# Kernel tuning notes

Hardware: AMD Instinct MI355X
Metric: run time of the kernel (lower is better)

Reference implementation:

```python
import jax, jax.numpy as jnp
import numpy as np

B, V, T, D, NC = 512, 4, 16, 512, 174
EPS = 1e-5
_edges = np.ones((V, V)) - np.eye(V)
SEND = np.where(_edges)[0]   # [12]
RECV = np.where(_edges)[1]   # [12]
E2N = jnp.asarray(np.eye(V)[RECV].T, dtype=jnp.float32)  # [V, E] one-hot recv matrix


def _bn(x, g, b):
    # BatchNorm1d in training mode: batch stats over flattened rows, biased var
    m = x.mean(axis=0)
    v = jnp.var(x, axis=0)
    return (x - m) * jax.lax.rsqrt(v + EPS) * g + b


def _mlp(x, w1, b1, w2, b2, g, bb):
    # RefNRIMLP: Linear-ELU-(Dropout p=0.1 disabled/eval)-Linear-ELU-BN
    h = jax.nn.elu(x @ w1 + b1)
    h = jax.nn.elu(h @ w2 + b2)
    return _bn(h, g, bb)


def setup_inputs() -> dict:
    key = jax.random.key(0)
    ks = iter(jax.random.split(key, 64))
    def W(*s):
        return jax.random.normal(next(ks), s, dtype=jnp.float32) * 0.02
    def zeros(*s):
        return jnp.zeros(s, jnp.float32)
    def ones(*s):
        return jnp.ones(s, jnp.float32)
    return dict(
        global_img_input=zeros(1),
        box_categories=jax.random.randint(next(ks), (B, T, V), 0, 3),
        box_input=jax.random.uniform(next(ks), (B, T, V, 4), dtype=jnp.float32),
        hand_id=jax.random.randint(next(ks), (B,), 0, 2),
        video_label=jax.random.randint(next(ks), (B,), 0, NC),
        emb=W(3, D // 2),
        c2f_w1=W(4, D // 2), c2f_g1=ones(D // 2), c2f_b1=zeros(D // 2),
        c2f_w2=W(D // 2, D), c2f_g2=ones(D), c2f_b2=zeros(D),
        fus_w=W(D + D // 2, D), fus_g=ones(D), fus_b=zeros(D),
        m1_w1=W(2 * D, D), m1_b1=zeros(D), m1_w2=W(D, D), m1_b2=zeros(D), m1_g=ones(D), m1_bb=zeros(D),
        m2_w1=W(D, D), m2_b1=zeros(D), m2_w2=W(D, D), m2_b2=zeros(D), m2_g=ones(D), m2_bb=zeros(D),
        t1_w1=W(2 * D, D), t1_b1=zeros(D), t1_w2=W(D, D), t1_b2=zeros(D), t1_g=ones(D), t1_bb=zeros(D),
        ps_w1=W(D, D), ps_g1=ones(D), ps_b1=zeros(D), ps_w2=W(D, D), ps_g2=ones(D), ps_b2=zeros(D),
        tb_w1=W(T * D, D), tb_g1=ones(D), tb_b1=zeros(D), tb_w2=W(D, D), tb_g2=ones(D), tb_b2=zeros(D),
        cl_w1=W(D, D), cl_b1=zeros(D), cl_w2=W(D, 512), cl_b2=zeros(512),
        cl_w3=W(512, NC), cl_b3=zeros(NC),
    )


def reference(global_img_input, box_categories, box_input, hand_id, video_label,
              emb, c2f_w1, c2f_g1, c2f_b1, c2f_w2, c2f_g2, c2f_b2,
              fus_w, fus_g, fus_b,
              m1_w1, m1_b1, m1_w2, m1_b2, m1_g, m1_bb,
              m2_w1, m2_b1, m2_w2, m2_b2, m2_g, m2_bb,
              t1_w1, t1_b1, t1_w2, t1_b2, t1_g, t1_bb,
              ps_w1, ps_g1, ps_b1, ps_w2, ps_g2, ps_b2,
              tb_w1, tb_g1, tb_b1, tb_w2, tb_g2, tb_b2,
              cl_w1, cl_b1, cl_w2, cl_b2, cl_w3, cl_b3):
    b = hand_id.shape[0]
    # [b,T,V,*] -> [b,V,T,*] -> flatten rows
    x = box_input.transpose(0, 2, 1, 3).reshape(-1, 4)          # [b*V*T, 4]
    cats = box_categories.transpose(0, 2, 1).reshape(-1)        # [b*V*T]
    pad_mask = (jnp.arange(3)[:, None] != 0).astype(emb.dtype)  # padding_idx=0
    ce = (emb * pad_mask)[cats]                                 # [b*V*T, D/2]
    # coord_to_feature: Linear(no bias)-BN-ReLU x2
    h = jax.nn.relu(_bn(x @ c2f_w1, c2f_g1, c2f_b1))
    h = jax.nn.relu(_bn(h @ c2f_w2, c2f_g2, c2f_b2))
    # coord_category_fusion
    bf = jax.nn.relu(_bn(jnp.concatenate([h, ce], axis=1) @ fus_w, fus_g, fus_b))
    bf = bf.reshape(b, V, T, D)
    # node2edge gather + mlp1
    e = jnp.concatenate([bf[:, SEND], bf[:, RECV]], axis=-1).reshape(-1, 2 * D)
    e = _mlp(e, m1_w1, m1_b1, m1_w2, m1_b2, m1_g, m1_bb).reshape(b, len(SEND), T, D)
    # edge2node: one-hot matmul aggregation / (V-1)
    n = jnp.einsum('ve,betd->bvtd', E2N, e) / (V - 1)
    n = _mlp(n.reshape(-1, D), m2_w1, m2_b1, m2_w2, m2_b2, m2_g, m2_bb).reshape(b, V, T, D)
    # temporal MLP on cat(node, bf)
    p = jnp.concatenate([n, bf], axis=-1).reshape(-1, 2 * D)
    p = _mlp(p, t1_w1, t1_b1, t1_w2, t1_b2, t1_g, t1_bb)
    # point_spatial_node_fusion
    p = jax.nn.relu(_bn(p @ ps_w1, ps_g1, ps_b1))
    p = jax.nn.relu(_bn(p @ ps_w2, ps_g2, ps_b2))
    # t_box_feature_fusion over flattened time
    q = p.reshape(b * V, T * D)
    q = jax.nn.relu(_bn(q @ tb_w1, tb_g1, tb_b1))
    q = jax.nn.relu(_bn(q @ tb_w2, tb_g2, tb_b2))
    feat = q.reshape(b, V, D).mean(axis=1)                      # mean over boxes
    h1 = jax.nn.relu(feat @ cl_w1 + cl_b1)
    h2 = jax.nn.relu(h1 @ cl_w2 + cl_b2)
    pf = h2 @ cl_w3 + cl_b3                                      # [b, NC]
    return (pf, video_label)
```

## Files before the change

kernel.cpp:

```cpp
#include <hip/hip_runtime.h>
#include <math.h>

#define EPS_ 1e-5f

static constexpr int Bb = 512, Vv = 4, Tt = 16, Dd = 512, NCc = 174;
static constexpr int NROW = Bb * Vv * Tt;
static constexpr int EROW = Bb * 12 * Tt;
static constexpr int CB = 128;
static constexpr int NCHUNK = Bb / CB;
static constexpr int CROWS_N = CB * Vv * Tt;
static constexpr int CROWS_E = CB * 12 * Tt;

__constant__ int d_SEND[12] = {0,0,0,1,1,1,2,2,2,3,3,3};
__constant__ int d_RECV[12] = {1,2,3,0,2,3,0,1,3,0,1,2};
__constant__ int d_EOFV[4][3] = {{3,6,9},{0,7,10},{1,4,11},{2,5,8}};

typedef float f32x4 __attribute__((ext_vector_type(4)));
typedef short s16x8 __attribute__((ext_vector_type(8)));

static __device__ __forceinline__ float b2f(unsigned short u) {
    union { unsigned int i; float f; } x; x.i = ((unsigned int)u) << 16; return x.f;
}
static __device__ __forceinline__ unsigned short f2b(float f) {
    union { float f; unsigned int i; } x; x.f = f;
    unsigned int r = (x.i + 0x7fffu + ((x.i >> 16) & 1u)) >> 16;
    return (unsigned short)r;
}
static __device__ __forceinline__ float act_f(float v, int act) {
    if (act == 1) return fmaxf(v, 0.f);
    if (act == 2) return (v > 0.f) ? v : (__expf(v) - 1.f);
    return v;
}

#define GL2LDS(g, l) __builtin_amdgcn_global_load_lds(                     \
    (__attribute__((address_space(1))) void*)(g),                          \
    (__attribute__((address_space(3))) void*)(l), 16, 0, 0)

#define CS_STRIDE 136

__global__ __launch_bounds__(256) void gemm_bf16(
    const unsigned short* __restrict__ A0, int Ka0, int K0,
    const unsigned short* __restrict__ A1, int Ka1, int K1,
    const unsigned short* __restrict__ WT, int Kw, int wtoff,
    unsigned short* __restrict__ C, int M, int N,
    const float* __restrict__ bias, int act,
    float* __restrict__ pstats, int accum,
    float* __restrict__ Cpart, int Ksl)
{
    __shared__ __align__(16) unsigned short SMEM[24576];
    int tid = threadIdx.x;
    int lane = tid & 63, wave = tid >> 6;
    int wr = wave >> 1, wc = wave & 1;
    int g = lane >> 4, r16 = lane & 15;

    int nct = N >> 7, nrt = M >> 7;
    int id = blockIdx.x, bx, by;
    if ((nrt & 7) == 0) {
        int grp = id / (nct * 8);
        int rem = id - grp * nct * 8;
        by = grp * 8 + (rem & 7);
        bx = rem >> 3;
    } else { bx = id % nct; by = id / nct; }
    int rowBase = by * 128;
    int colBase = bx * 128;
    int koff = blockIdx.z * Ksl;

    int srow = wave * 32 + (lane >> 2);
    int scol = (lane & 3) * 8;
    const unsigned short* wrow  = WT + (size_t)(colBase + srow) * Kw + wtoff + scol;
    const unsigned short* wrow2 = WT + (size_t)(colBase + srow + 16) * Kw + wtoff + scol;

    f32x4 acc[4][4];
#pragma unroll
    for (int i = 0; i < 4; ++i)
#pragma unroll
        for (int j = 0; j < 4; ++j) acc[i][j] = (f32x4){0.f, 0.f, 0.f, 0.f};

#define STAGE_(kg_, SL_) do {                                                   \
        int kg = (kg_);                                                         \
        const unsigned short* Ap; int lda; int kc;                              \
        if (kg < K0) { Ap = A0; lda = Ka0; kc = kg; }                           \
        else         { Ap = A1; lda = Ka1; kc = kg - K0; }                      \
        const unsigned short* ga = Ap + (size_t)(rowBase + srow) * lda + kc + scol; \
        GL2LDS(ga, (SL_) + wave * 1024);                                        \
        GL2LDS(ga + (size_t)16 * lda, (SL_) + wave * 1024 + 512);               \
        GL2LDS(wrow + kg, (SL_) + 4096 + wave * 1024);                          \
        GL2LDS(wrow2 + kg, (SL_) + 4096 + wave * 1024 + 512);                   \
    } while (0)

    int nt = Ksl >> 5;
    STAGE_(koff, SMEM);
    if (nt > 1) STAGE_(koff + 32, SMEM + 8192);
    int cur = 0;
    for (int t = 0; t < nt; ++t) {
        if (t + 1 < nt) asm volatile("s_waitcnt vmcnt(4)" ::: "memory");
        else            asm volatile("s_waitcnt vmcnt(0)" ::: "memory");
        __builtin_amdgcn_s_barrier();
        __builtin_amdgcn_sched_barrier(0);
        if (t + 2 < nt) {
            int nx = cur + 2; if (nx >= 3) nx -= 3;
            STAGE_(koff + (t + 2) * 32, SMEM + nx * 8192);
        }
        unsigned short* SA = SMEM + cur * 8192;
        unsigned short* SB = SA + 4096;
        s16x8 xf[4], wf[4];
#pragma unroll
        for (int j = 0; j < 4; ++j)
            xf[j] = *(const s16x8*)(SA + (wr * 64 + j * 16 + r16) * 32 + g * 8);
#pragma unroll
        for (int i = 0; i < 4; ++i)
            wf[i] = *(const s16x8*)(SB + (wc * 64 + i * 16 + r16) * 32 + g * 8);
#pragma unroll
        for (int i = 0; i < 4; ++i)
#pragma unroll
            for (int j = 0; j < 4; ++j)
                acc[i][j] = __builtin_amdgcn_mfma_f32_16x16x32_bf16(
                    wf[i], xf[j], acc[i][j], 0, 0, 0);
        cur = (cur == 2) ? 0 : cur + 1;
    }
#undef STAGE_
    __syncthreads();

    if (Cpart) {
#pragma unroll
        for (int j = 0; j < 4; ++j) {
            int row = rowBase + wr * 64 + j * 16 + r16;
#pragma unroll
            for (int i = 0; i < 4; ++i) {
                int col0 = colBase + wc * 64 + i * 16 + g * 4;
                float4 v = make_float4(acc[i][j][0], acc[i][j][1],
                                       acc[i][j][2], acc[i][j][3]);
                *(float4*)&Cpart[((size_t)blockIdx.z * M + row) * N + col0] = v;
            }
        }
        return;
    }

#pragma unroll
    for (int i = 0; i < 4; ++i) {
        int lc0 = wc * 64 + i * 16 + g * 4;
        float4 b4 = bias ? *(const float4*)(bias + colBase + lc0)
                         : make_float4(0.f, 0.f, 0.f, 0.f);
        float s[4] = {0.f, 0.f, 0.f, 0.f}, q[4] = {0.f, 0.f, 0.f, 0.f};
#pragma unroll
        for (int j = 0; j < 4; ++j) {
            int lr = wr * 64 + j * 16 + r16;
            float v0 = act_f(acc[i][j][0] + b4.x, act);
            float v1 = act_f(acc[i][j][1] + b4.y, act);
            float v2 = act_f(acc[i][j][2] + b4.z, act);
            float v3 = act_f(acc[i][j][3] + b4.w, act);
            *(ushort4*)&SMEM[lr * CS_STRIDE + lc0] =
                make_ushort4(f2b(v0), f2b(v1), f2b(v2), f2b(v3));
            s[0] += v0; s[1] += v1; s[2] += v2; s[3] += v3;
            q[0] += v0 * v0; q[1] += v1 * v1; q[2] += v2 * v2; q[3] += v3 * v3;
        }
        if (pstats) {
#pragma unroll
            for (int p = 0; p < 4; ++p) {
#pragma unroll
                for (int d = 1; d < 16; d <<= 1) {
                    s[p] += __shfl_xor(s[p], d);
                    q[p] += __shfl_xor(q[p], d);
                }
            }
            if (r16 == 0) {
                float* pr = pstats + ((size_t)(by * 2 + wr)) * 1024 + colBase + lc0;
                float4 s4 = make_float4(s[0], s[1], s[2], s[3]);
                float4 q4 = make_float4(q[0], q[1], q[2], q[3]);
                if (accum) {
                    float4 o = *(float4*)pr;
                    s4.x += o.x; s4.y += o.y; s4.z += o.z; s4.w += o.w;
                    float4 o2 = *(float4*)(pr + 512);
                    q4.x += o2.x; q4.y += o2.y; q4.z += o2.z; q4.w += o2.w;
                }
                *(float4*)pr = s4;
                *(float4*)(pr + 512) = q4;
            }
        }
    }
    __syncthreads();
    {
        int qd = tid & 3;
        int rr = tid >> 2;
#pragma unroll
        for (int pass = 0; pass < 2; ++pass) {
            int lr = pass * 64 + rr;
            size_t grow = (size_t)(rowBase + lr) * N + colBase;
#pragma unroll
            for (int u = 0; u < 4; ++u) {
                int cofs = u * 32 + qd * 8;
                uint4 v = *(const uint4*)(SMEM + lr * CS_STRIDE + cofs);
                *(uint4*)&C[grow + cofs] = v;
            }
        }
    }
}

__global__ __launch_bounds__(256) void finalize_stats_k(
    const float* __restrict__ P, int nrows, float* __restrict__ slot)
{
    __shared__ float red[256];
    int lane = threadIdx.x & 63;
    int seg  = threadIdx.x >> 6;
    int col  = blockIdx.x * 64 + lane;
    float s = 0.f;
    for (int r = seg; r < nrows; r += 4)
        s += P[(size_t)r * 1024 + col];
    red[threadIdx.x] = s;
    __syncthreads();
    if (seg == 0)
        slot[col] = red[lane] + red[64 + lane] + red[128 + lane] + red[192 + lane];
}

__global__ __launch_bounds__(256) void fold_bn_k(
    const float* __restrict__ slot, const float* __restrict__ gm,
    const float* __restrict__ bt, float inv_cnt, float premul,
    unsigned short* __restrict__ WT, int Kw, int kof,
    const float* __restrict__ Wsrc, const float* __restrict__ bias_in,
    float* __restrict__ bias_out)
{
    int blk = blockIdx.x;
    if (blk < 1024) {
        int i = blk * 256 + threadIdx.x;
        int n = i >> 9, k = i & 511;
        float mean = slot[k] * inv_cnt;
        float var = fmaxf(slot[512 + k] * inv_cnt - mean * mean, 0.f);
        float sc = gm[k] * rsqrtf(var + EPS_) * premul;
        unsigned short* p = &WT[(size_t)n * Kw + kof + k];
        *p = f2b(b2f(*p) * sc);
    } else {
        __shared__ float red[256];
        int blk2 = blk - 1024;
        int lane = threadIdx.x & 63;
        int seg  = threadIdx.x >> 6;
        int n = blk2 * 64 + lane;
        float acc = 0.f;
        int k0 = seg * 128;
#pragma unroll 4
        for (int k = k0; k < k0 + 128; ++k) {
            float mean = slot[k] * inv_cnt;
            float var = fmaxf(slot[512 + k] * inv_cnt - mean * mean, 0.f);
            float sc = gm[k] * rsqrtf(var + EPS_);
            float sh = bt[k] - mean * sc;
            acc += sh * Wsrc[(size_t)k * 512 + n];
        }
        red[threadIdx.x] = acc;
        __syncthreads();
        if (seg == 0)
            bias_out[n] = (bias_in ? bias_in[n] : 0.f)
                        + red[lane] + red[64 + lane]
                        + red[128 + lane] + red[192 + lane];
    }
}

__global__ __launch_bounds__(256) void combine_k(
    const float4* __restrict__ P, int S, int M,
    unsigned short* __restrict__ C, float* __restrict__ pstats, int act)
{
    int col4 = threadIdx.x & 127;
    int rh = threadIdx.x >> 7;
    int rb = blockIdx.y * 8;
    float4 s4 = make_float4(0.f, 0.f, 0.f, 0.f);
    float4 q4 = make_float4(0.f, 0.f, 0.f, 0.f);
#pragma unroll
    for (int i = 0; i < 4; ++i) {
        int row = rb + rh + 2 * i;
        float4 v = make_float4(0.f, 0.f, 0.f, 0.f);
#pragma unroll
        for (int z = 0; z < 8; ++z) {
            float4 p = P[((size_t)z * M + row) * 128 + col4];
            v.x += p.x; v.y += p.y; v.z += p.z; v.w += p.w;
        }
        v.x = act_f(v.x, act); v.y = act_f(v.y, act);
        v.z = act_f(v.z, act); v.w = act_f(v.w, act);
        ((ushort4*)C)[(size_t)row * 128 + col4] =
            make_ushort4(f2b(v.x), f2b(v.y), f2b(v.z), f2b(v.w));
        s4.x += v.x; s4.y += v.y; s4.z += v.z; s4.w += v.w;
        q4.x += v.x * v.x; q4.y += v.y * v.y; q4.z += v.z * v.z; q4.w += v.w * v.w;
    }
    __shared__ float4 sb[256], qb[256];
    sb[threadIdx.x] = s4; qb[threadIdx.x] = q4;
    __syncthreads();
    if (threadIdx.x < 128) {
        float4 a = sb[threadIdx.x], b = sb[threadIdx.x + 128];
        float4 c = qb[threadIdx.x], d = qb[threadIdx.x + 128];
        int col = threadIdx.x * 4;
        float* pr = pstats + (size_t)blockIdx.y * 1024 + col;
        *(float4*)pr = make_float4(a.x + b.x, a.y + b.y, a.z + b.z, a.w + b.w);
        *(float4*)(pr + 512) = make_float4(c.x + d.x, c.y + d.y, c.z + d.z, c.w + d.w);
    }
}

#define NTD 13
struct TBatch {
    const float* src[NTD];
    unsigned short* dst[NTD];
    int K[NTD];
    int tbase[NTD + 1];
};
__global__ __launch_bounds__(256) void transpose_batch_k(TBatch tb)
{
    int id = blockIdx.x;
    int d = 0;
#pragma unroll
    for (int j = 0; j < NTD; ++j) if (id >= tb.tbase[j + 1]) d = j + 1;
    int rel = id - tb.tbase[d];
    int kt = rel >> 3, ntl = rel & 7;
    int k0 = kt * 64, n0 = ntl * 64;
    const float* S = tb.src[d];
    unsigned short* D = tb.dst[d];
    int K = tb.K[d];
    __shared__ unsigned short L[64][68];
    int c = threadIdx.x & 63;
    int r = threadIdx.x >> 6;
#pragma unroll
    for (int p = 0; p < 16; ++p) {
        int kk = r + p * 4;
        L[kk][c] = f2b(S[(size_t)(k0 + kk) * 512 + n0 + c]);
    }
    __syncthreads();
#pragma unroll
    for (int p = 0; p < 16; ++p) {
        int nn = r + p * 4;
        D[(size_t)(n0 + nn) * K + k0 + c] = L[c][nn];
    }
}

__global__ __launch_bounds__(256) void transpose_pq_k(
    const float* __restrict__ W, unsigned short* __restrict__ WT)
{
    int id = blockIdx.x;
    int kt = id >> 4, ntl = id & 15;
    int k0 = kt * 64, n0 = ntl * 64;
    __shared__ unsigned short L[64][68];
    int c = threadIdx.x & 63;
    int r = threadIdx.x >> 6;
    int nb = n0 + c;
    const float* S = (n0 < 512) ? (W + nb) : (W + (size_t)512 * 512 + (nb - 512));
#pragma unroll
    for (int p = 0; p < 16; ++p) {
        int kk = r + p * 4;
        L[kk][c] = f2b(S[(size_t)(k0 + kk) * 512]);
    }
    __syncthreads();
#pragma unroll
    for (int p = 0; p < 16; ++p) {
        int nn = r + p * 4;
        WT[(size_t)(n0 + nn) * 512 + k0 + c] = L[c][nn];
    }
}

__global__ __launch_bounds__(256) void colstats_k(
    const unsigned short* __restrict__ X, float* __restrict__ P)
{
    __shared__ float sb[256][4], qb[256][4];
    int c4 = threadIdx.x & 63;
    int seg = threadIdx.x >> 6;
    int r0 = blockIdx.x * 128;
    float s[4] = {0.f, 0.f, 0.f, 0.f}, q[4] = {0.f, 0.f, 0.f, 0.f};
    for (int r = r0 + seg; r < r0 + 128; r += 4) {
        ushort4 x = ((const ushort4*)X)[(size_t)r * 64 + c4];
        float v0 = b2f(x.x), v1 = b2f(x.y), v2 = b2f(x.z), v3 = b2f(x.w);
        s[0] += v0; s[1] += v1; s[2] += v2; s[3] += v3;
        q[0] += v0 * v0; q[1] += v1 * v1; q[2] += v2 * v2; q[3] += v3 * v3;
    }
#pragma unroll
    for (int e = 0; e < 4; ++e) { sb[threadIdx.x][e] = s[e]; qb[threadIdx.x][e] = q[e]; }
    __syncthreads();
    if (threadIdx.x < 64) {
        int c = threadIdx.x;
        float4 S, Q;
        S.x = sb[c][0] + sb[c + 64][0] + sb[c + 128][0] + sb[c + 192][0];
        S.y = sb[c][1] + sb[c + 64][1] + sb[c + 128][1] + sb[c + 192][1];
        S.z = sb[c][2] + sb[c + 64][2] + sb[c + 128][2] + sb[c + 192][2];
        S.w = sb[c][3] + sb[c + 64][3] + sb[c + 128][3] + sb[c + 192][3];
        Q.x = qb[c][0] + qb[c + 64][0] + qb[c + 128][0] + qb[c + 192][0];
        Q.y = qb[c][1] + qb[c + 64][1] + qb[c + 128][1] + qb[c + 192][1];
        Q.z = qb[c][2] + qb[c + 64][2] + qb[c + 128][2] + qb[c + 192][2];
        Q.w = qb[c][3] + qb[c + 64][3] + qb[c + 128][3] + qb[c + 192][3];
        *(float4*)&P[(size_t)blockIdx.x * 1024 + c * 4] = S;
        *(float4*)&P[(size_t)blockIdx.x * 1024 + 512 + c * 4] = Q;
    }
}

__global__ __launch_bounds__(256) void bn_apply_k(
    unsigned short* __restrict__ X, long n4, int cmask4, int C,
    const float* __restrict__ slot, const float* __restrict__ gm,
    const float* __restrict__ bt, float inv_cnt, float premul, int act)
{
    __shared__ float sc_s[512], sh_s[512];
    for (int c = threadIdx.x; c < C; c += 256) {
        float mean = slot[c] * inv_cnt;
        float var = fmaxf(slot[512 + c] * inv_cnt - mean * mean, 0.f);
        float sc = gm[c] * rsqrtf(var + EPS_);
        sc_s[c] = sc * premul;
        sh_s[c] = bt[c] - mean * sc;
    }
    __syncthreads();
    long stride = (long)gridDim.x * 256;
    for (long i = (long)blockIdx.x * 256 + threadIdx.x; i < n4; i += stride) {
        ushort4 x = ((ushort4*)X)[i];
        int c = ((int)(i & cmask4)) * 4;
        unsigned short o[4] = {x.x, x.y, x.z, x.w};
#pragma unroll
        for (int e = 0; e < 4; ++e) {
            float v = b2f(o[e]) * sc_s[c + e] + sh_s[c + e];
            o[e] = f2b(act_f(v, act));
        }
        ((ushort4*)X)[i] = make_ushort4(o[0], o[1], o[2], o[3]);
    }
}

__global__ __launch_bounds__(256) void zero_k(float* p, int n)
{
    int i = blockIdx.x * 256 + threadIdx.x;
    if (i < n) p[i] = 0.f;
}

__global__ __launch_bounds__(256) void build_x0_k(
    const float* __restrict__ box, float* __restrict__ X0)
{
    int i = blockIdx.x * 256 + threadIdx.x;
    if (i >= NROW * 4) return;
    int c = i & 3; int r = i >> 2;
    int t = r & 15; int bv = r >> 4; int v = bv & 3; int b = bv >> 2;
    X0[i] = box[(((size_t)b * Tt + t) * Vv + v) * 4 + c];
}

__global__ __launch_bounds__(256) void build_ce_k(
    const int* __restrict__ cats, const float* __restrict__ emb,
    unsigned short* __restrict__ CE)
{
    int i = blockIdx.x * 256 + threadIdx.x;
    if (i >= NROW * 64) return;
    int c4 = i & 63; int r = i >> 6;
    int t = r & 15; int bv = r >> 4; int v = bv & 3; int b = bv >> 2;
    int cat = cats[((size_t)b * Tt + t) * Vv + v];
    unsigned short o[4];
#pragma unroll
    for (int e = 0; e < 4; ++e)
        o[e] = (cat == 0) ? 0 : f2b(emb[cat * 256 + c4 * 4 + e]);
    ((ushort4*)CE)[(size_t)r * 64 + c4] = make_ushort4(o[0], o[1], o[2], o[3]);
}

__global__ __launch_bounds__(256) void smallk_gemm_k(
    const float* __restrict__ X0, const float* __restrict__ W4,
    unsigned short* __restrict__ Y1)
{
    int i = blockIdx.x * 256 + threadIdx.x;
    if (i >= NROW * 64) return;
    int n4 = i & 63; int m = i >> 6;
    float4 x = *(const float4*)(X0 + m * 4);
    unsigned short o[4];
#pragma unroll
    for (int e = 0; e < 4; ++e) {
        int n = n4 * 4 + e;
        float v = x.x * W4[n] + x.y * W4[256 + n] + x.z * W4[512 + n] + x.w * W4[768 + n];
        o[e] = f2b(v);
    }
    ((ushort4*)Y1)[(size_t)m * 64 + n4] = make_ushort4(o[0], o[1], o[2], o[3]);
}

__global__ __launch_bounds__(256) void edge_gather_k(
    const unsigned short* __restrict__ PQ,
    const float* __restrict__ b1, unsigned short* __restrict__ E)
{
    int i = blockIdx.x * 256 + threadIdx.x;
    if (i >= CROWS_E * 128) return;
    int c4 = i & 127; int m = i >> 7;
    int t = m & 15; int be = m >> 4; int e = be % 12; int brel = be / 12;
    int s = d_SEND[e], r = d_RECV[e];
    ushort4 p = ((const ushort4*)PQ)[(((size_t)brel * 4 + s) * 16 + t) * 256 + c4];
    ushort4 q = ((const ushort4*)PQ)[(((size_t)brel * 4 + r) * 16 + t) * 256 + 128 + c4];
    unsigned short pa[4] = {p.x, p.y, p.z, p.w}, qa[4] = {q.x, q.y, q.z, q.w}, o[4];
#pragma unroll
    for (int e2 = 0; e2 < 4; ++e2) {
        float v = b2f(pa[e2]) + b2f(qa[e2]) + b1[c4 * 4 + e2];
        o[e2] = f2b(act_f(v, 2));
    }
    ((ushort4*)E)[i] = make_ushort4(o[0], o[1], o[2], o[3]);
}

__global__ __launch_bounds__(256) void edge_agg_k(
    const unsigned short* __restrict__ E2c, unsigned short* __restrict__ nraw, int b0)
{
    int i = blockIdx.x * 256 + threadIdx.x;
    if (i >= CB * Vv * Tt * 128) return;
    int c4 = i & 127; int r = i >> 7;
    int t = r & 15; int r2 = r >> 4; int v = r2 & 3; int brel = r2 >> 2;
    float s[4] = {0.f, 0.f, 0.f, 0.f};
#pragma unroll
    for (int j = 0; j < 3; ++j) {
        int e = d_EOFV[v][j];
        ushort4 x = ((const ushort4*)E2c)[(((size_t)brel * 12 + e) * 16 + t) * 128 + c4];
        s[0] += b2f(x.x); s[1] += b2f(x.y); s[2] += b2f(x.z); s[3] += b2f(x.w);
    }
    ((ushort4*)nraw)[((((size_t)(b0 + brel)) * 4 + v) * 16 + t) * 128 + c4] =
        make_ushort4(f2b(s[0]), f2b(s[1]), f2b(s[2]), f2b(s[3]));
}

__global__ __launch_bounds__(256) void feat_mean_k(
    const unsigned short* __restrict__ q, unsigned short* __restrict__ feat)
{
    int i = blockIdx.x * 256 + threadIdx.x;
    if (i >= Bb * 128) return;
    int c4 = i & 127; int b = i >> 7;
    float s[4] = {0.f, 0.f, 0.f, 0.f};
#pragma unroll
    for (int v = 0; v < 4; ++v) {
        ushort4 x = ((const ushort4*)q)[(((size_t)b * 4 + v)) * 128 + c4];
        s[0] += b2f(x.x); s[1] += b2f(x.y); s[2] += b2f(x.z); s[3] += b2f(x.w);
    }
    ((ushort4*)feat)[(size_t)b * 128 + c4] = make_ushort4(
        f2b(0.25f * s[0]), f2b(0.25f * s[1]), f2b(0.25f * s[2]), f2b(0.25f * s[3]));
}

__global__ __launch_bounds__(256) void final_gemm_k(
    const unsigned short* __restrict__ H2, const float* __restrict__ W,
    const float* __restrict__ b, float* __restrict__ out)
{
    __shared__ float Ls[4 * 512];
    int m0 = blockIdx.x * 4;
    for (int i = threadIdx.x; i < 512; i += 256) {
        ushort4 x = ((const ushort4*)H2)[(size_t)m0 * 128 + i];
        *(float4*)&Ls[i * 4] = make_float4(b2f(x.x), b2f(x.y), b2f(x.z), b2f(x.w));
    }
    __syncthreads();
    int n = threadIdx.x;
    if (n >= NCc) return;
    float a0 = b[n], a1 = a0, a2 = a0, a3 = a0;
#pragma unroll 8
    for (int k = 0; k < 512; ++k) {
        float w = W[(size_t)k * NCc + n];
        a0 += Ls[k] * w;
        a1 += Ls[512 + k] * w;
        a2 += Ls[1024 + k] * w;
        a3 += Ls[1536 + k] * w;
    }
    out[(size_t)m0 * NCc + n] = a0;
    out[(size_t)(m0 + 1) * NCc + n] = a1;
    out[(size_t)(m0 + 2) * NCc + n] = a2;
    out[(size_t)(m0 + 3) * NCc + n] = a3;
}

__global__ __launch_bounds__(256) void copy_labels_k(
    const int* __restrict__ lab, float* __restrict__ out)
{
    int i = blockIdx.x * 256 + threadIdx.x;
    if (i < Bb) out[i] = (float)lab[i];
}

static inline void gemm(hipStream_t s,
                        const unsigned short* A0, int Ka0, int K0,
                        const unsigned short* A1, int Ka1, int K1,
                        const unsigned short* WT, int Kw, int wtoff,
                        unsigned short* C, int M, int N,
                        const float* bias, int act, float* pstats, int accum)
{
    dim3 g((N / 128) * (M / 128), 1, 1);
    hipLaunchKernelGGL(gemm_bf16, g, dim3(256), 0, s,
                       A0, Ka0, K0, A1, Ka1, K1, WT, Kw, wtoff, C, M, N,
                       bias, act, pstats, accum, (float*)nullptr, K0 + K1);
}

static inline void finalize(hipStream_t s, const float* P, int nrows, float* slot)
{
    hipLaunchKernelGGL(finalize_stats_k, dim3(16), dim3(256), 0, s, P, nrows, slot);
}

static inline void bn_apply(hipStream_t s, unsigned short* X, long n, int C,
                            const float* slot, const float* gm, const float* bt,
                            float cnt, float premul, int act)
{
    long n4 = n / 4;
    long nb = (n4 + 255) / 256;
    if (nb > 1024) nb = 1024;
    hipLaunchKernelGGL(bn_apply_k, dim3((unsigned)nb), dim3(256), 0, s,
                       X, n4, C / 4 - 1, C, slot, gm, bt, 1.f / cnt, premul, act);
}

static inline void fold_bn(hipStream_t s, const float* slot, const float* gm,
                           const float* bt, float cnt, float premul,
                           unsigned short* WT, int Kw, int kof,
                           const float* Wsrc, const float* bias_in, float* bias_out)
{
    hipLaunchKernelGGL(fold_bn_k, dim3(1032), dim3(256), 0, s,
                       slot, gm, bt, 1.f / cnt, premul, WT, Kw, kof,
                       Wsrc, bias_in, bias_out);
}

extern "C" void kernel_launch(void* const* d_in, const int* in_sizes, int n_in,
                              void* d_out, int out_size, void* d_ws, size_t ws_size,
                              hipStream_t stream)
{
    const int*   box_cat = (const int*)  d_in[1];
    const float* box_in  = (const float*)d_in[2];
    const int*   vlabel  = (const int*)  d_in[4];
    const float* emb     = (const float*)d_in[5];
    const float* c2f_w1  = (const float*)d_in[6];
    const float* c2f_g1  = (const float*)d_in[7];
    const float* c2f_b1  = (const float*)d_in[8];
    const float* c2f_w2  = (const float*)d_in[9];
    const float* c2f_g2  = (const float*)d_in[10];
    const float* c2f_b2  = (const float*)d_in[11];
    const float* fus_w   = (const float*)d_in[12];
    const float* fus_g   = (const float*)d_in[13];
    const float* fus_b   = (const float*)d_in[14];
    const float* m1_w1   = (const float*)d_in[15];
    const float* m1_b1   = (const float*)d_in[16];
    const float* m1_w2   = (const float*)d_in[17];
    const float* m1_b2   = (const float*)d_in[18];
    const float* m1_g    = (const float*)d_in[19];
    const float* m1_bb   = (const float*)d_in[20];
    const float* m2_w1   = (const float*)d_in[21];
    const float* m2_b1   = (const float*)d_in[22];
    const float* m2_w2   = (const float*)d_in[23];
    const float* m2_b2   = (const float*)d_in[24];
    const float* m2_g    = (const float*)d_in[25];
    const float* m2_bb   = (const float*)d_in[26];
    const float* t1_w1   = (const float*)d_in[27];
    const float* t1_b1   = (const float*)d_in[28];
    const float* t1_w2   = (const float*)d_in[29];
    const float* t1_b2   = (const float*)d_in[30];
    const float* t1_g    = (const float*)d_in[31];
    const float* t1_bb   = (const float*)d_in[32];
    const float* ps_w1   = (const float*)d_in[33];
    const float* ps_g1   = (const float*)d_in[34];
    const float* ps_b1   = (const float*)d_in[35];
    const float* ps_w2   = (const float*)d_in[36];
    const float* ps_g2   = (const float*)d_in[37];
    const float* ps_b2   = (const float*)d_in[38];
    const float* tb_w1   = (const float*)d_in[39];
    const float* tb_g1   = (const float*)d_in[40];
    const float* tb_b1   = (const float*)d_in[41];
    const float* tb_w2   = (const float*)d_in[42];
    const float* tb_g2   = (const float*)d_in[43];
    const float* tb_b2   = (const float*)d_in[44];
    const float* cl_w1   = (const float*)d_in[45];
    const float* cl_b1   = (const float*)d_in[46];
    const float* cl_w2   = (const float*)d_in[47];
    const float* cl_b2   = (const float*)d_in[48];
    const float* cl_w3   = (const float*)d_in[49];
    const float* cl_b3   = (const float*)d_in[50];

    float* out = (float*)d_out;

    char* base = (char*)d_ws;
    const size_t SZ_ACT = (size_t)NROW * 512 * 2;
    unsigned short* A0v = (unsigned short*)(base);
    unsigned short* A1v = (unsigned short*)(base + SZ_ACT);
    char* Sreg = base + 2 * SZ_ACT;
    unsigned short* A2v = (unsigned short*)Sreg;
    unsigned short* CE  = (unsigned short*)Sreg;
    unsigned short* Y1  = (unsigned short*)(Sreg + (size_t)NROW * 256 * 2);
    unsigned short* PQc = (unsigned short*)Sreg;
    unsigned short* EC1 = (unsigned short*)(Sreg + (size_t)CROWS_N * 1024 * 2);
    unsigned short* EC2 = (unsigned short*)(Sreg + (size_t)CROWS_N * 1024 * 2
                                                 + (size_t)CROWS_E * 512 * 2);
    float* Ppart = (float*)Sreg;
    char* wtb = Sreg + (size_t)CROWS_N * 1024 * 2 + 2 * (size_t)CROWS_E * 512 * 2;
    unsigned short* wtp = (unsigned short*)wtb;
    size_t wo = 0;
    auto alloc_wt = [&](int K) { unsigned short* p = wtp + wo; wo += (size_t)K * 512; return p; };
    unsigned short* WTc2f2 = alloc_wt(256);
    unsigned short* WTfus  = alloc_wt(768);
    unsigned short* WTpq   = alloc_wt(1024);
    unsigned short* WTm1b  = alloc_wt(512);
    unsigned short* WTm2a  = alloc_wt(512);
    unsigned short* WTm2b  = alloc_wt(512);
    unsigned short* WTt1a  = alloc_wt(1024);
    unsigned short* WTt1b  = alloc_wt(512);
    unsigned short* WTps1  = alloc_wt(512);
    unsigned short* WTps2  = alloc_wt(512);
    unsigned short* WTtb1  = alloc_wt(8192);
    unsigned short* WTtb2  = alloc_wt(512);
    unsigned short* WTcl1  = alloc_wt(512);
    unsigned short* WTcl2  = alloc_wt(512);
    float* X0f    = (float*)(wtp + wo);
    float* STATS  = X0f + (size_t)NROW * 4;
    float* PSTATS = STATS + 10 * 1024;
    float* BIASF  = PSTATS + 512 * 1024;

    auto slot = [&](int i) { return STATS + (size_t)i * 1024; };

    {
        int nz = 10 * 1024 + 384 * 1024;
        hipLaunchKernelGGL(zero_k, dim3((nz + 255) / 256), dim3(256), 0, stream,
                           STATS, nz);
    }
    {
        TBatch tb;
        const float* srcs[NTD] = {c2f_w2, fus_w, m1_w2, m2_w1, m2_w2, t1_w1, t1_w2,
                                  ps_w1, ps_w2, tb_w1, tb_w2, cl_w1, cl_w2};
        unsigned short* dsts[NTD] = {WTc2f2, WTfus, WTm1b, WTm2a, WTm2b, WTt1a, WTt1b,
                                     WTps1, WTps2, WTtb1, WTtb2, WTcl1, WTcl2};
        int Ks[NTD] = {256, 768, 512, 512, 512, 1024, 512, 512, 512, 8192, 512, 512, 512};
        int acc = 0;
        for (int i = 0; i < NTD; ++i) {
            tb.src[i] = srcs[i]; tb.dst[i] = dsts[i]; tb.K[i] = Ks[i];
            tb.tbase[i] = acc; acc += (Ks[i] / 64) * 8;
        }
        tb.tbase[NTD] = acc;
        hipLaunchKernelGGL(transpose_batch_k, dim3((unsigned)acc), dim3(256), 0,
                           stream, tb);
    }
    hipLaunchKernelGGL(transpose_pq_k, dim3(128), dim3(256), 0, stream, m1_w1, WTpq);

    hipLaunchKernelGGL(build_x0_k, dim3((NROW * 4 + 255) / 256), dim3(256), 0, stream,
                       box_in, X0f);
    hipLaunchKernelGGL(build_ce_k, dim3((NROW * 64 + 255) / 256), dim3(256), 0, stream,
                       box_cat, emb, CE);

    hipLaunchKernelGGL(smallk_gemm_k, dim3((NROW * 64 + 255) / 256), dim3(256), 0,
                       stream, X0f, c2f_w1, Y1);
    hipLaunchKernelGGL(colstats_k, dim3(NROW / 128), dim3(256), 0, stream, Y1, PSTATS);
    finalize(stream, PSTATS, NROW / 128, slot(0));
    bn_apply(stream, Y1, (long)NROW * 256, 256, slot(0), c2f_g1, c2f_b1,
             (float)NROW, 1.f, 1);

    gemm(stream, Y1, 256, 256, nullptr, 0, 0, WTc2f2, 256, 0, A1v, NROW, 512,
         nullptr, 0, PSTATS, 0);
    finalize(stream, PSTATS, 512, slot(1));
    bn_apply(stream, A1v, (long)NROW * 512, 512, slot(1), c2f_g2, c2f_b2,
             (float)NROW, 1.f, 1);

    gemm(stream, A1v, 512, 512, CE, 256, 256, WTfus, 768, 0, A0v, NROW, 512,
         nullptr, 0, PSTATS, 0);
    finalize(stream, PSTATS, 512, slot(2));
    bn_apply(stream, A0v, (long)NROW * 512, 512, slot(2), fus_g, fus_b,
             (float)NROW, 1.f, 1);

    for (int c = 0; c < NCHUNK; ++c) {
        const unsigned short* BFc = A0v + (size_t)c * CROWS_N * 512;
        gemm(stream, BFc, 512, 512, nullptr, 0, 0, WTpq, 512, 0, PQc, CROWS_N, 1024,
             nullptr, 0, nullptr, 0);
        hipLaunchKernelGGL(edge_gather_k, dim3((CROWS_E * 128 + 255) / 256), dim3(256),
                           0, stream, PQc, m1_b1, EC1);
        gemm(stream, EC1, 512, 512, nullptr, 0, 0, WTm1b, 512, 0, EC2, CROWS_E, 512,
             m1_b2, 2, PSTATS, 1);
        hipLaunchKernelGGL(edge_agg_k, dim3((CB * Vv * Tt * 128 + 255) / 256), dim3(256),
                           0, stream, EC2, A1v, c * CB);
    }
    finalize(stream, PSTATS, 384, slot(3));
    fold_bn(stream, slot(3), m1_g, m1_bb, (float)EROW, 1.f / 3.f,
            WTm2a, 512, 0, m2_w1, m2_b1, BIASF);

    gemm(stream, A1v, 512, 512, nullptr, 0, 0, WTm2a, 512, 0, A2v, NROW, 512,
         BIASF, 2, nullptr, 0);
    gemm(stream, A2v, 512, 512, nullptr, 0, 0, WTm2b, 512, 0, A1v, NROW, 512,
         m2_b2, 2, PSTATS, 0);
    finalize(stream, PSTATS, 512, slot(4));
    fold_bn(stream, slot(4), m2_g, m2_bb, (float)NROW, 1.f,
            WTt1a, 1024, 0, t1_w1, t1_b1, BIASF + 512);

    gemm(stream, A1v, 512, 512, A0v, 512, 512, WTt1a, 1024, 0, A2v, NROW, 512,
         BIASF + 512, 2, nullptr, 0);
    gemm(stream, A2v, 512, 512, nullptr, 0, 0, WTt1b, 512, 0, A1v, NROW, 512,
         t1_b2, 2, PSTATS, 0);
    finalize(stream, PSTATS, 512, slot(5));
    fold_bn(stream, slot(5), t1_g, t1_bb, (float)NROW, 1.f,
            WTps1, 512, 0, ps_w1, nullptr, BIASF + 1024);

    gemm(stream, A1v, 512, 512, nullptr, 0, 0, WTps1, 512, 0, A2v, NROW, 512,
         BIASF + 1024, 0, PSTATS, 0);
    finalize(stream, PSTATS, 512, slot(6));
    bn_apply(stream, A2v, (long)NROW * 512, 512, slot(6), ps_g1, ps_b1,
             (float)NROW, 1.f, 1);

    gemm(stream, A2v, 512, 512, nullptr, 0, 0, WTps2, 512, 0, A0v, NROW, 512,
         nullptr, 0, PSTATS, 0);
    finalize(stream, PSTATS, 512, slot(7));
    bn_apply(stream, A0v, (long)NROW * 512, 512, slot(7), ps_g2, ps_b2,
             (float)NROW, 1.f, 1);

    {
        dim3 g((512 / 128) * (2048 / 128), 1, 8);
        hipLaunchKernelGGL(gemm_bf16, g, dim3(256), 0, stream,
                           A0v, 8192, 8192, (const unsigned short*)nullptr, 0, 0,
                           WTtb1, 8192, 0, A1v, 2048, 512,
                           (const float*)nullptr, 0, (float*)nullptr, 0, Ppart, 1024);
        hipLaunchKernelGGL(combine_k, dim3(1, 2048 / 8), dim3(256), 0, stream,
                           (const float4*)Ppart, 8, 2048, A1v, PSTATS, 0);
        finalize(stream, PSTATS, 2048 / 8, slot(8));
    }
    bn_apply(stream, A1v, (long)Bb * Vv * 512, 512, slot(8), tb_g1, tb_b1,
             (float)(Bb * Vv), 1.f, 1);

    gemm(stream, A1v, 512, 512, nullptr, 0, 0, WTtb2, 512, 0, A2v, Bb * Vv, 512,
         nullptr, 0, PSTATS, 0);
    finalize(stream, PSTATS, (Bb * Vv / 128) * 2, slot(9));
    bn_apply(stream, A2v, (long)Bb * Vv * 512, 512, slot(9), tb_g2, tb_b2,
             (float)(Bb * Vv), 1.f, 1);

    hipLaunchKernelGGL(feat_mean_k, dim3((Bb * 128 + 255) / 256), dim3(256), 0, stream,
                       A2v, A0v);

    gemm(stream, A0v, 512, 512, nullptr, 0, 0, WTcl1, 512, 0, A1v, Bb, 512,
         cl_b1, 1, nullptr, 0);
    gemm(stream, A1v, 512, 512, nullptr, 0, 0, WTcl2, 512, 0, A2v, Bb, 512,
         cl_b2, 1, nullptr, 0);
    hipLaunchKernelGGL(final_gemm_k, dim3(Bb / 4), dim3(256), 0, stream,
                       A2v, cl_w3, cl_b3, out);

    hipLaunchKernelGGL(copy_labels_k, dim3((Bb + 255) / 256), dim3(256), 0, stream,
                       vlabel, out + (size_t)Bb * NCc);
}
```

Measured before the change: 1.256 ms.

## Use BK=64 double-buffered GEMM with XOR-swizzled LDS layout

Changes the bf16 GEMM main loop from a 3-stage pipeline with K-step 32 to a 2-stage double buffer with K-step 64, and adds an XOR swizzle on the LDS layout so fragment reads avoid bank conflicts. The aim is to halve the barriers per K and cut LDS bank conflicts. In exchange, LDS per block grows to 64KB, which may lower occupancy, and the fine-grained vmcnt waits are replaced by full __syncthreads. Any split-K slice length must now be a multiple of 64.

```diff
diff --git a/kernel.cpp b/kernel.cpp
--- a/kernel.cpp
+++ b/kernel.cpp
@@ -47,7 +47,7 @@
     float* __restrict__ pstats, int accum,
     float* __restrict__ Cpart, int Ksl)
 {
-    __shared__ __align__(16) unsigned short SMEM[24576];
+    __shared__ __align__(16) unsigned short SMEM[32768];
     int tid = threadIdx.x;
     int lane = tid & 63, wave = tid >> 6;
     int wr = wave >> 1, wc = wave & 1;
@@ -65,10 +65,8 @@
     int colBase = bx * 128;
     int koff = blockIdx.z * Ksl;
 
-    int srow = wave * 32 + (lane >> 2);
-    int scol = (lane & 3) * 8;
-    const unsigned short* wrow  = WT + (size_t)(colBase + srow) * Kw + wtoff + scol;
-    const unsigned short* wrow2 = WT + (size_t)(colBase + srow + 16) * Kw + wtoff + scol;
+    int sr8 = lane >> 3;
+    int gsw = ((lane & 7) ^ sr8) << 3;
 
     f32x4 acc[4][4];
 #pragma unroll
@@ -81,45 +79,52 @@
         const unsigned short* Ap; int lda; int kc;                              \
         if (kg < K0) { Ap = A0; lda = Ka0; kc = kg; }                           \
         else         { Ap = A1; lda = Ka1; kc = kg - K0; }                      \
-        const unsigned short* ga = Ap + (size_t)(rowBase + srow) * lda + kc + scol; \
-        GL2LDS(ga, (SL_) + wave * 1024);                                        \
-        GL2LDS(ga + (size_t)16 * lda, (SL_) + wave * 1024 + 512);               \
-        GL2LDS(wrow + kg, (SL_) + 4096 + wave * 1024);                          \
-        GL2LDS(wrow2 + kg, (SL_) + 4096 + wave * 1024 + 512);                   \
+        const unsigned short* ga = Ap + (size_t)(rowBase + wave * 32 + sr8) * lda \
+                                      + kc + gsw;                               \
+        const unsigned short* gb = WT + (size_t)(colBase + wave * 32 + sr8) * Kw \
+                                      + wtoff + kg + gsw;                       \
+        unsigned short* la = (SL_) + wave * 2048;                               \
+        unsigned short* lb = (SL_) + 8192 + wave * 2048;                        \
+        GL2LDS(ga, la);                                                         \
+        GL2LDS(ga + (size_t)8 * lda, la + 512);                                 \
+        GL2LDS(ga + (size_t)16 * lda, la + 1024);                               \
+        GL2LDS(ga + (size_t)24 * lda, la + 1536);                               \
+        GL2LDS(gb, lb);                                                         \
+        GL2LDS(gb + (size_t)8 * Kw, lb + 512);                                  \
+        GL2LDS(gb + (size_t)16 * Kw, lb + 1024);                                \
+        GL2LDS(gb + (size_t)24 * Kw, lb + 1536);                                \
     } while (0)
 
-    int nt = Ksl >> 5;
+    int nt = Ksl >> 6;
     STAGE_(koff, SMEM);
-    if (nt > 1) STAGE_(koff + 32, SMEM + 8192);
-    int cur = 0;
+    __syncthreads();
+    int rsw = r16 & 7;
     for (int t = 0; t < nt; ++t) {
-        if (t + 1 < nt) asm volatile("s_waitcnt vmcnt(4)" ::: "memory");
-        else            asm volatile("s_waitcnt vmcnt(0)" ::: "memory");
-        __builtin_amdgcn_s_barrier();
-        __builtin_amdgcn_sched_barrier(0);
-        if (t + 2 < nt) {
-            int nx = cur + 2; if (nx >= 3) nx -= 3;
-            STAGE_(koff + (t + 2) * 32, SMEM + nx * 8192);
+        unsigned short* SL = SMEM + (t & 1) * 16384;
+        if (t + 1 < nt)
+            STAGE_(koff + (t + 1) * 64, SMEM + ((t & 1) ^ 1) * 16384);
+        unsigned short* SA = SL;
+        unsigned short* SB = SL + 8192;
+#pragma unroll
+        for (int kk = 0; kk < 2; ++kk) {
+            int gr = ((kk * 4 + g) ^ rsw) << 3;
+            s16x8 xf[4], wf[4];
+#pragma unroll
+            for (int j = 0; j < 4; ++j)
+                xf[j] = *(const s16x8*)(SA + (wr * 64 + j * 16 + r16) * 64 + gr);
+#pragma unroll
+            for (int i = 0; i < 4; ++i)
+                wf[i] = *(const s16x8*)(SB + (wc * 64 + i * 16 + r16) * 64 + gr);
+#pragma unroll
+            for (int i = 0; i < 4; ++i)
+#pragma unroll
+                for (int j = 0; j < 4; ++j)
+                    acc[i][j] = __builtin_amdgcn_mfma_f32_16x16x32_bf16(
+                        wf[i], xf[j], acc[i][j], 0, 0, 0);
         }
-        unsigned short* SA = SMEM + cur * 8192;
-        unsigned short* SB = SA + 4096;
-        s16x8 xf[4], wf[4];
-#pragma unroll
-        for (int j = 0; j < 4; ++j)
-            xf[j] = *(const s16x8*)(SA + (wr * 64 + j * 16 + r16) * 32 + g * 8);
-#pragma unroll
-        for (int i = 0; i < 4; ++i)
-            wf[i] = *(const s16x8*)(SB + (wc * 64 + i * 16 + r16) * 32 + g * 8);
-#pragma unroll
-        for (int i = 0; i < 4; ++i)
-#pragma unroll
-            for (int j = 0; j < 4; ++j)
-                acc[i][j] = __builtin_amdgcn_mfma_f32_16x16x32_bf16(
-                    wf[i], xf[j], acc[i][j], 0, 0, 0);
-        cur = (cur == 2) ? 0 : cur + 1;
+        __syncthreads();
     }
 #undef STAGE_
-    __syncthreads();
 
     if (Cpart) {
 #pragma unroll
```

New measurement: 1.273 ms. About the same (+1.4%).
